# Optimization experiments

Measured on AMD Instinct MI355X. Metric: run time of the kernel, lower is better.

Reference implementation:

```python
import jax, jax.numpy as jnp
import numpy as np

N_NODES = 50000
N_EDGES = 800000
IN_SIZE = 128
HIDDEN = 128   # out_size * 2
OUT_SIZE = 64


def setup_inputs() -> dict:
    key = jax.random.key(0)
    ks = jax.random.split(key, 6)
    h = jax.random.normal(ks[0], (N_NODES, IN_SIZE), dtype=jnp.float32)
    W1 = jax.random.normal(ks[1], (IN_SIZE, HIDDEN), dtype=jnp.float32) * (1.0 / np.sqrt(IN_SIZE))
    b1 = jnp.zeros((HIDDEN,), dtype=jnp.float32)
    W2 = jax.random.normal(ks[2], (HIDDEN, OUT_SIZE), dtype=jnp.float32) * (1.0 / np.sqrt(HIDDEN))
    b2 = jnp.zeros((OUT_SIZE,), dtype=jnp.float32)
    src = jax.random.randint(ks[3], (N_EDGES,), 0, N_NODES, dtype=jnp.int64)
    dst = jax.random.randint(ks[4], (N_EDGES,), 0, N_NODES, dtype=jnp.int64)
    return {"h": h, "W1": W1, "b1": b1, "W2": W2, "b2": b2, "src": src, "dst": dst}


def _norms(src, dst, n_nodes):
    # DGL GraphConv norm='both': scale by out_degree^{-1/2} (src side)
    # and in_degree^{-1/2} (dst side); zero degrees clamped to 1.
    ones = jnp.ones(src.shape, dtype=jnp.float32)
    out_deg = jnp.maximum(jax.ops.segment_sum(ones, src, num_segments=n_nodes), 1.0)
    in_deg = jnp.maximum(jax.ops.segment_sum(ones, dst, num_segments=n_nodes), 1.0)
    return (out_deg ** -0.5)[:, None], (in_deg ** -0.5)[:, None]


def _graph_conv(x, W, b, src, dst, norm_out, norm_in, n_nodes):
    # h' = D_in^{-1/2} A D_out^{-1/2} x W + b
    x = x * norm_out                                   # [N, F]
    agg = jax.ops.segment_sum(x[src], dst, num_segments=n_nodes)  # SpMM: [N, F]
    return (agg * norm_in) @ W + b


def reference(h, W1, b1, W2, b2, src, dst):
    n_nodes = h.shape[0]
    norm_out, norm_in = _norms(src, dst, n_nodes)
    h = jax.nn.relu(_graph_conv(h, W1, b1, src, dst, norm_out, norm_in, n_nodes))
    h = jax.nn.relu(_graph_conv(h, W2, b2, src, dst, norm_out, norm_in, n_nodes))
    return h
```

## Files before the change

### kernel.cpp

```cpp
#include <hip/hip_runtime.h>

#define N_NODES 50000
#define N_EDGES 800000
#define IN_SIZE 128
#define HIDDEN 128
#define OUT_SIZE 64

#define CHUNKS 128
#define CHUNK_EDGES 6250
#define NBS 196
#define GA_BLOCKS 391

typedef __attribute__((ext_vector_type(8))) short bf16x8;
typedef __attribute__((ext_vector_type(4))) float f32x4;

static __device__ inline unsigned short bf16_rne(float x) {
    unsigned ua = __float_as_uint(x);
    return (unsigned short)((ua + 0x7fffu + ((ua >> 16) & 1u)) >> 16);
}

static __device__ inline unsigned short f16_bits(float x) {
    _Float16 hx = (_Float16)x;
    return __builtin_bit_cast(unsigned short, hx);
}

static __device__ inline unsigned pack_f16x2(float a, float b) {
    return (unsigned)f16_bits(a) | ((unsigned)f16_bits(b) << 16);
}

static __device__ inline float2 unpack_f16x2(unsigned u) {
    _Float16 lo = __builtin_bit_cast(_Float16, (unsigned short)(u & 0xffffu));
    _Float16 hi = __builtin_bit_cast(_Float16, (unsigned short)(u >> 16));
    return make_float2((float)lo, (float)hi);
}

__global__ __launch_bounds__(256) void wpack_kernel(const float* __restrict__ W1,
                                                    const float* __restrict__ W2,
                                                    unsigned short* __restrict__ wf_hi,
                                                    unsigned short* __restrict__ wf_lo,
                                                    unsigned short* __restrict__ wf2_hi,
                                                    unsigned short* __restrict__ wf2_lo) {
    int idx = blockIdx.x * 256 + threadIdx.x;
    if (idx < 2048) {
        int l  = idx & 63;
        int ct = (idx >> 6) & 7;
        int ks = idx >> 9;
        int col = ct * 16 + (l & 15);
        int k0  = ks * 32 + (l >> 4) * 8;
        unsigned short hi[8], lo[8];
        #pragma unroll
        for (int j = 0; j < 8; ++j) {
            float x = W1[(size_t)(k0 + j) * 128 + col];
            unsigned short h16 = bf16_rne(x);
            hi[j] = h16;
            lo[j] = bf16_rne(x - __uint_as_float((unsigned)h16 << 16));
        }
        ((uint4*)wf_hi)[idx] = *(const uint4*)hi;
        ((uint4*)wf_lo)[idx] = *(const uint4*)lo;
    } else if (idx < 3072) {
        int i2 = idx - 2048;
        int l  = i2 & 63;
        int ct = (i2 >> 6) & 3;
        int ks = i2 >> 8;
        int col = ct * 16 + (l & 15);
        int k0  = ks * 32 + (l >> 4) * 8;
        unsigned short hi[8], lo[8];
        #pragma unroll
        for (int j = 0; j < 8; ++j) {
            float x = W2[(size_t)(k0 + j) * 64 + col];
            unsigned short h16 = bf16_rne(x);
            hi[j] = h16;
            lo[j] = bf16_rne(x - __uint_as_float((unsigned)h16 << 16));
        }
        ((uint4*)wf2_hi)[i2] = *(const uint4*)hi;
        ((uint4*)wf2_lo)[i2] = *(const uint4*)lo;
    }
}

__global__ __launch_bounds__(256) void gemmA_kernel(const float* __restrict__ h,
                                                    const unsigned short* __restrict__ wf_hi,
                                                    const unsigned short* __restrict__ wf_lo,
                                                    const float* __restrict__ norm_out,
                                                    unsigned short* __restrict__ t1) {
    const int t  = threadIdx.x;
    const int wv = t >> 6;
    const int l  = t & 63;
    const int lrow = l & 15;
    const int g    = l >> 4;
    const int n0 = blockIdx.x * 128 + wv * 32;

    int r0 = n0 + lrow;      if (r0 > N_NODES - 1) r0 = N_NODES - 1;
    int r1 = n0 + 16 + lrow; if (r1 > N_NODES - 1) r1 = N_NODES - 1;
    const float* h0 = h + (size_t)r0 * 128 + g * 8;
    const float* h1 = h + (size_t)r1 * 128 + g * 8;

    f32x4 acc[2][8];
    #pragma unroll
    for (int rt = 0; rt < 2; ++rt)
        #pragma unroll
        for (int ct = 0; ct < 8; ++ct)
            acc[rt][ct] = (f32x4){0.f, 0.f, 0.f, 0.f};

    const bf16x8* bh_base = (const bf16x8*)wf_hi;
    const bf16x8* bl_base = (const bf16x8*)wf_lo;

    for (int ks = 0; ks < 4; ++ks) {
        float a0[8], a1[8];
        *(float4*)(a0)     = *(const float4*)(h0 + ks * 32);
        *(float4*)(a0 + 4) = *(const float4*)(h0 + ks * 32 + 4);
        *(float4*)(a1)     = *(const float4*)(h1 + ks * 32);
        *(float4*)(a1 + 4) = *(const float4*)(h1 + ks * 32 + 4);

        bf16x8 a0h, a0l, a1h, a1l;
        #pragma unroll
        for (int j = 0; j < 8; ++j) {
            unsigned short hh = bf16_rne(a0[j]);
            a0h[j] = (short)hh;
            a0l[j] = (short)bf16_rne(a0[j] - __uint_as_float((unsigned)hh << 16));
            unsigned short h2 = bf16_rne(a1[j]);
            a1h[j] = (short)h2;
            a1l[j] = (short)bf16_rne(a1[j] - __uint_as_float((unsigned)h2 << 16));
        }

        #pragma unroll
        for (int ct = 0; ct < 8; ++ct) {
            const int fi = (ks * 8 + ct) * 64 + l;
            bf16x8 bh = bh_base[fi];
            bf16x8 bl = bl_base[fi];
            acc[0][ct] = __builtin_amdgcn_mfma_f32_16x16x32_bf16(a0l, bh, acc[0][ct], 0, 0, 0);
            acc[0][ct] = __builtin_amdgcn_mfma_f32_16x16x32_bf16(a0h, bl, acc[0][ct], 0, 0, 0);
            acc[0][ct] = __builtin_amdgcn_mfma_f32_16x16x32_bf16(a0h, bh, acc[0][ct], 0, 0, 0);
            acc[1][ct] = __builtin_amdgcn_mfma_f32_16x16x32_bf16(a1l, bh, acc[1][ct], 0, 0, 0);
            acc[1][ct] = __builtin_amdgcn_mfma_f32_16x16x32_bf16(a1h, bl, acc[1][ct], 0, 0, 0);
            acc[1][ct] = __builtin_amdgcn_mfma_f32_16x16x32_bf16(a1h, bh, acc[1][ct], 0, 0, 0);
        }
    }

    #pragma unroll
    for (int rt = 0; rt < 2; ++rt) {
        float no_[4];
        #pragma unroll
        for (int r = 0; r < 4; ++r) {
            int row = n0 + rt * 16 + g * 4 + r;
            no_[r] = (row < N_NODES) ? norm_out[row] : 0.f;
        }
        #pragma unroll
        for (int ct = 0; ct < 8; ++ct) {
            #pragma unroll
            for (int r = 0; r < 4; ++r) {
                int row = n0 + rt * 16 + g * 4 + r;
                if (row < N_NODES)
                    t1[(size_t)row * 128 + ct * 16 + lrow] = bf16_rne(acc[rt][ct][r] * no_[r]);
            }
        }
    }
}

__global__ __launch_bounds__(256) void gemmB_kernel(const float* __restrict__ h1p,
                                                    const unsigned short* __restrict__ wf2_hi,
                                                    const unsigned short* __restrict__ wf2_lo,
                                                    unsigned short* __restrict__ t2h) {
    const int t  = threadIdx.x;
    const int wv = t >> 6;
    const int l  = t & 63;
    const int lrow = l & 15;
    const int g    = l >> 4;
    const int n0 = blockIdx.x * 128 + wv * 32;

    int r0 = n0 + lrow;      if (r0 > N_NODES - 1) r0 = N_NODES - 1;
    int r1 = n0 + 16 + lrow; if (r1 > N_NODES - 1) r1 = N_NODES - 1;
    const float* h0 = h1p + (size_t)r0 * 128 + g * 8;
    const float* h1 = h1p + (size_t)r1 * 128 + g * 8;

    f32x4 acc[2][4];
    #pragma unroll
    for (int rt = 0; rt < 2; ++rt)
        #pragma unroll
        for (int ct = 0; ct < 4; ++ct)
            acc[rt][ct] = (f32x4){0.f, 0.f, 0.f, 0.f};

    const bf16x8* bh_base = (const bf16x8*)wf2_hi;
    const bf16x8* bl_base = (const bf16x8*)wf2_lo;

    for (int ks = 0; ks < 4; ++ks) {
        float a0[8], a1[8];
        *(float4*)(a0)     = *(const float4*)(h0 + ks * 32);
        *(float4*)(a0 + 4) = *(const float4*)(h0 + ks * 32 + 4);
        *(float4*)(a1)     = *(const float4*)(h1 + ks * 32);
        *(float4*)(a1 + 4) = *(const float4*)(h1 + ks * 32 + 4);

        bf16x8 a0h, a0l, a1h, a1l;
        #pragma unroll
        for (int j = 0; j < 8; ++j) {
            unsigned short hh = bf16_rne(a0[j]);
            a0h[j] = (short)hh;
            a0l[j] = (short)bf16_rne(a0[j] - __uint_as_float((unsigned)hh << 16));
            unsigned short h2 = bf16_rne(a1[j]);
            a1h[j] = (short)h2;
            a1l[j] = (short)bf16_rne(a1[j] - __uint_as_float((unsigned)h2 << 16));
        }

        #pragma unroll
        for (int ct = 0; ct < 4; ++ct) {
            const int fi = (ks * 4 + ct) * 64 + l;
            bf16x8 bh = bh_base[fi];
            bf16x8 bl = bl_base[fi];
            acc[0][ct] = __builtin_amdgcn_mfma_f32_16x16x32_bf16(a0l, bh, acc[0][ct], 0, 0, 0);
            acc[0][ct] = __builtin_amdgcn_mfma_f32_16x16x32_bf16(a0h, bl, acc[0][ct], 0, 0, 0);
            acc[0][ct] = __builtin_amdgcn_mfma_f32_16x16x32_bf16(a0h, bh, acc[0][ct], 0, 0, 0);
            acc[1][ct] = __builtin_amdgcn_mfma_f32_16x16x32_bf16(a1l, bh, acc[1][ct], 0, 0, 0);
            acc[1][ct] = __builtin_amdgcn_mfma_f32_16x16x32_bf16(a1h, bl, acc[1][ct], 0, 0, 0);
            acc[1][ct] = __builtin_amdgcn_mfma_f32_16x16x32_bf16(a1h, bh, acc[1][ct], 0, 0, 0);
        }
    }

    #pragma unroll
    for (int rt = 0; rt < 2; ++rt) {
        #pragma unroll
        for (int ct = 0; ct < 4; ++ct) {
            #pragma unroll
            for (int r = 0; r < 4; ++r) {
                int row = n0 + rt * 16 + g * 4 + r;
                if (row < N_NODES)
                    t2h[(size_t)row * 64 + ct * 16 + lrow] = f16_bits(acc[rt][ct][r]);
            }
        }
    }
}

__global__ __launch_bounds__(1024) void hist_kernel(const int* __restrict__ src,
                                                    const int* __restrict__ dst,
                                                    unsigned char* __restrict__ cntD,
                                                    unsigned char* __restrict__ cntS,
                                                    unsigned char* __restrict__ rp) {
    __shared__ unsigned hD[12500];
    __shared__ unsigned hS[12500];
    const int t = threadIdx.x;
    const int c = blockIdx.x;

    for (int i = t; i < 12500; i += 1024) { hD[i] = 0u; hS[i] = 0u; }
    __syncthreads();

    const int base = c * CHUNK_EDGES;
    for (int i = t; i < CHUNK_EDGES; i += 1024) {
        int e = base + i;
        int d = dst[e];
        int s = src[e];
        unsigned shd = (unsigned)(d & 3) * 8u;
        unsigned old = atomicAdd(&hD[d >> 2], 1u << shd);
        rp[e] = (unsigned char)((old >> shd) & 0xffu);
        atomicAdd(&hS[s >> 2], 1u << ((unsigned)(s & 3) * 8u));
    }
    __syncthreads();

    unsigned* gD = (unsigned*)cntD + (size_t)c * 12500;
    unsigned* gS = (unsigned*)cntS + (size_t)c * 12500;
    for (int i = t; i < 12500; i += 1024) { gD[i] = hD[i]; gS[i] = hS[i]; }
}

__global__ __launch_bounds__(256) void deg_scan_kernel(unsigned char* __restrict__ cntD,
                                                       const unsigned char* __restrict__ cntS,
                                                       int* __restrict__ row_ptr,
                                                       int* __restrict__ bsum,
                                                       float* __restrict__ norm_out,
                                                       float* __restrict__ norm_in) {
    const int t = threadIdx.x, lane = t & 63, w = t >> 6;
    const int n = blockIdx.x * 256 + t;
    unsigned sumD = 0u, sumS = 0u;
    if (n < N_NODES) {
        #pragma unroll 4
        for (int c = 0; c < CHUNKS; ++c) {
            size_t idx = (size_t)c * 50000 + n;
            unsigned v = cntD[idx];
            cntD[idx] = (unsigned char)sumD;
            sumD += v;
            sumS += cntS[idx];
        }
        norm_in[n]  = rsqrtf((float)(sumD ? sumD : 1u));
        norm_out[n] = rsqrtf((float)(sumS ? sumS : 1u));
    }
    __shared__ int wsum[4];
    int v = (n < N_NODES) ? (int)sumD : 0;
    int incl = v;
    #pragma unroll
    for (int d = 1; d < 64; d <<= 1) {
        int u = __shfl_up(incl, d, 64);
        if (lane >= d) incl += u;
    }
    if (lane == 63) wsum[w] = incl;
    __syncthreads();
    int woff = 0, total = 0;
    #pragma unroll
    for (int j = 0; j < 4; ++j) {
        int s = wsum[j];
        if (j < w) woff += s;
        total += s;
    }
    if (n < N_NODES) row_ptr[n] = woff + incl - v;
    if (t == 0) bsum[blockIdx.x] = total;
}

__global__ __launch_bounds__(64) void scan2_kernel(int* __restrict__ bsum,
                                                   int* __restrict__ row_ptr) {
    const int lane = threadIdx.x;
    int carry = 0;
    for (int base = 0; base < NBS; base += 64) {
        int t = base + lane;
        int v = (t < NBS) ? bsum[t] : 0;
        int incl = v;
        #pragma unroll
        for (int d = 1; d < 64; d <<= 1) {
            int u = __shfl_up(incl, d, 64);
            if (lane >= d) incl += u;
        }
        int excl = carry + incl - v;
        if (t < NBS) bsum[t] = excl;
        if (t == NBS - 1) row_ptr[N_NODES] = N_EDGES - excl;
        carry += __shfl(incl, 63, 64);
    }
}

__global__ __launch_bounds__(256) void place_kernel(const int* __restrict__ src,
                                                    const int* __restrict__ dst,
                                                    const int* __restrict__ row_ptr,
                                                    const int* __restrict__ bsum,
                                                    const unsigned char* __restrict__ cntD,
                                                    const unsigned char* __restrict__ rp,
                                                    int* __restrict__ eidx) {
    int e = blockIdx.x * 256 + threadIdx.x;
    if (e < N_EDGES) {
        int d = dst[e];
        int c = e / CHUNK_EDGES;
        int pos = row_ptr[d] + bsum[d >> 8] + (int)cntD[(size_t)c * 50000 + d] + (int)rp[e];
        eidx[pos] = src[e];
    }
}

__global__ __launch_bounds__(256) void pull128_kernel(const unsigned short* __restrict__ xb,
                                                      const int* __restrict__ row_ptr,
                                                      const int* __restrict__ bsum,
                                                      const int* __restrict__ eidx,
                                                      const float* __restrict__ b1,
                                                      const float* __restrict__ norm_in,
                                                      const float* __restrict__ norm_out,
                                                      float* __restrict__ out) {
    int node = blockIdx.x * 4 + (threadIdx.x >> 6);
    node = __builtin_amdgcn_readfirstlane(node);
    const int lane = threadIdx.x & 63;
    const int beg = __builtin_amdgcn_readfirstlane(row_ptr[node] + bsum[node >> 8]);
    const int end = __builtin_amdgcn_readfirstlane(row_ptr[node + 1] + bsum[(node + 1) >> 8]);

    float2 acc0 = make_float2(0.f, 0.f);
    float2 acc1 = make_float2(0.f, 0.f);
    float2 acc2 = make_float2(0.f, 0.f);
    float2 acc3 = make_float2(0.f, 0.f);

    for (int base = beg; base < end; base += 64) {
        const int cnt = min(64, end - base);
        int my_e = (lane < cnt) ? eidx[base + lane] : 0;
        int k = 0;
        for (; k + 7 < cnt; k += 8) {
            int s0 = __builtin_amdgcn_readlane(my_e, k);
            int s1 = __builtin_amdgcn_readlane(my_e, k + 1);
            int s2 = __builtin_amdgcn_readlane(my_e, k + 2);
            int s3 = __builtin_amdgcn_readlane(my_e, k + 3);
            int s4 = __builtin_amdgcn_readlane(my_e, k + 4);
            int s5 = __builtin_amdgcn_readlane(my_e, k + 5);
            int s6 = __builtin_amdgcn_readlane(my_e, k + 6);
            int s7 = __builtin_amdgcn_readlane(my_e, k + 7);
            unsigned u0 = ((const unsigned*)(xb + (size_t)s0 * 128))[lane];
            unsigned u1 = ((const unsigned*)(xb + (size_t)s1 * 128))[lane];
            unsigned u2 = ((const unsigned*)(xb + (size_t)s2 * 128))[lane];
            unsigned u3 = ((const unsigned*)(xb + (size_t)s3 * 128))[lane];
            unsigned u4 = ((const unsigned*)(xb + (size_t)s4 * 128))[lane];
            unsigned u5 = ((const unsigned*)(xb + (size_t)s5 * 128))[lane];
            unsigned u6 = ((const unsigned*)(xb + (size_t)s6 * 128))[lane];
            unsigned u7 = ((const unsigned*)(xb + (size_t)s7 * 128))[lane];
            acc0.x += __uint_as_float(u0 << 16);
            acc0.y += __uint_as_float(u0 & 0xffff0000u);
            acc1.x += __uint_as_float(u1 << 16);
            acc1.y += __uint_as_float(u1 & 0xffff0000u);
            acc2.x += __uint_as_float(u2 << 16);
            acc2.y += __uint_as_float(u2 & 0xffff0000u);
            acc3.x += __uint_as_float(u3 << 16);
            acc3.y += __uint_as_float(u3 & 0xffff0000u);
            acc0.x += __uint_as_float(u4 << 16);
            acc0.y += __uint_as_float(u4 & 0xffff0000u);
            acc1.x += __uint_as_float(u5 << 16);
            acc1.y += __uint_as_float(u5 & 0xffff0000u);
            acc2.x += __uint_as_float(u6 << 16);
            acc2.y += __uint_as_float(u6 & 0xffff0000u);
            acc3.x += __uint_as_float(u7 << 16);
            acc3.y += __uint_as_float(u7 & 0xffff0000u);
        }
        for (; k + 3 < cnt; k += 4) {
            int s0 = __builtin_amdgcn_readlane(my_e, k);
            int s1 = __builtin_amdgcn_readlane(my_e, k + 1);
            int s2 = __builtin_amdgcn_readlane(my_e, k + 2);
            int s3 = __builtin_amdgcn_readlane(my_e, k + 3);
            unsigned u0 = ((const unsigned*)(xb + (size_t)s0 * 128))[lane];
            unsigned u1 = ((const unsigned*)(xb + (size_t)s1 * 128))[lane];
            unsigned u2 = ((const unsigned*)(xb + (size_t)s2 * 128))[lane];
            unsigned u3 = ((const unsigned*)(xb + (size_t)s3 * 128))[lane];
            acc0.x += __uint_as_float(u0 << 16);
            acc0.y += __uint_as_float(u0 & 0xffff0000u);
            acc1.x += __uint_as_float(u1 << 16);
            acc1.y += __uint_as_float(u1 & 0xffff0000u);
            acc2.x += __uint_as_float(u2 << 16);
            acc2.y += __uint_as_float(u2 & 0xffff0000u);
            acc3.x += __uint_as_float(u3 << 16);
            acc3.y += __uint_as_float(u3 & 0xffff0000u);
        }
        for (; k < cnt; ++k) {
            int s0 = __builtin_amdgcn_readlane(my_e, k);
            unsigned u0 = ((const unsigned*)(xb + (size_t)s0 * 128))[lane];
            acc0.x += __uint_as_float(u0 << 16);
            acc0.y += __uint_as_float(u0 & 0xffff0000u);
        }
    }

    float ni = norm_in[node];
    float no = norm_out[node];
    float2 bb = ((const float2*)b1)[lane];
    float sx = (acc0.x + acc1.x) + (acc2.x + acc3.x);
    float sy = (acc0.y + acc1.y) + (acc2.y + acc3.y);
    float2 r;
    r.x = fmaxf(fmaf(sx, ni, bb.x), 0.f) * no;
    r.y = fmaxf(fmaf(sy, ni, bb.y), 0.f) * no;
    ((float2*)(out + (size_t)node * 128))[lane] = r;
}

__global__ __launch_bounds__(256) void pull64_kernel(const unsigned* __restrict__ x,
                                                     const int* __restrict__ row_ptr,
                                                     const int* __restrict__ bsum,
                                                     const int* __restrict__ eidx,
                                                     const float* __restrict__ b2,
                                                     const float* __restrict__ norm_in,
                                                     float* __restrict__ out) {
    int node = blockIdx.x * 4 + (threadIdx.x >> 6);
    node = __builtin_amdgcn_readfirstlane(node);
    const int lane = threadIdx.x & 63;
    const int half = lane >> 5;
    const int fl = lane & 31;
    const int beg = __builtin_amdgcn_readfirstlane(row_ptr[node] + bsum[node >> 8]);
    const int end = __builtin_amdgcn_readfirstlane(row_ptr[node + 1] + bsum[(node + 1) >> 8]);

    float2 a0 = make_float2(0.f, 0.f);
    float2 a1 = make_float2(0.f, 0.f);
    float2 a2 = make_float2(0.f, 0.f);
    float2 a3 = make_float2(0.f, 0.f);

    for (int base = beg; base < end; base += 64) {
        const int cnt = min(64, end - base);
        int my_e = (lane < cnt) ? eidx[base + lane] : 0;
        int k = 0;
        for (; k + 7 < cnt; k += 8) {
            int sa0 = __builtin_amdgcn_readlane(my_e, k);
            int sb0 = __builtin_amdgcn_readlane(my_e, k + 1);
            int sa1 = __builtin_amdgcn_readlane(my_e, k + 2);
            int sb1 = __builtin_amdgcn_readlane(my_e, k + 3);
            int sa2 = __builtin_amdgcn_readlane(my_e, k + 4);
            int sb2 = __builtin_amdgcn_readlane(my_e, k + 5);
            int sa3 = __builtin_amdgcn_readlane(my_e, k + 6);
            int sb3 = __builtin_amdgcn_readlane(my_e, k + 7);
            int e0 = half ? sb0 : sa0;
            int e1 = half ? sb1 : sa1;
            int e2 = half ? sb2 : sa2;
            int e3 = half ? sb3 : sa3;
            unsigned u0 = x[(size_t)e0 * 32 + fl];
            unsigned u1 = x[(size_t)e1 * 32 + fl];
            unsigned u2 = x[(size_t)e2 * 32 + fl];
            unsigned u3 = x[(size_t)e3 * 32 + fl];
            float2 v0 = unpack_f16x2(u0);
            float2 v1 = unpack_f16x2(u1);
            float2 v2 = unpack_f16x2(u2);
            float2 v3 = unpack_f16x2(u3);
            a0.x += v0.x; a0.y += v0.y;
            a1.x += v1.x; a1.y += v1.y;
            a2.x += v2.x; a2.y += v2.y;
            a3.x += v3.x; a3.y += v3.y;
        }
        for (; k + 1 < cnt; k += 2) {
            int sa = __builtin_amdgcn_readlane(my_e, k);
            int sb = __builtin_amdgcn_readlane(my_e, k + 1);
            int e0 = half ? sb : sa;
            unsigned u = x[(size_t)e0 * 32 + fl];
            float2 v = unpack_f16x2(u);
            a0.x += v.x; a0.y += v.y;
        }
        if (k < cnt) {
            int sa = __builtin_amdgcn_readlane(my_e, k);
            if (half == 0) {
                unsigned u = x[(size_t)sa * 32 + fl];
                float2 v = unpack_f16x2(u);
                a0.x += v.x; a0.y += v.y;
            }
        }
    }

    float ax = (a0.x + a1.x) + (a2.x + a3.x);
    float ay = (a0.y + a1.y) + (a2.y + a3.y);
    ax += __shfl_xor(ax, 32, 64);
    ay += __shfl_xor(ay, 32, 64);
    if (half == 0) {
        float ni = norm_in[node];
        float2 bb = ((const float2*)b2)[fl];
        float2 r;
        r.x = fmaxf(fmaf(ax, ni, bb.x), 0.f);
        r.y = fmaxf(fmaf(ay, ni, bb.y), 0.f);
        ((float2*)(out + (size_t)node * 64))[fl] = r;
    }
}

extern "C" void kernel_launch(void* const* d_in, const int* in_sizes, int n_in,
                              void* d_out, int out_size, void* d_ws, size_t ws_size,
                              hipStream_t stream) {
    const float* h  = (const float*)d_in[0];
    const float* W1 = (const float*)d_in[1];
    const float* b1 = (const float*)d_in[2];
    const float* W2 = (const float*)d_in[3];
    const float* b2 = (const float*)d_in[4];
    const int* src  = (const int*)d_in[5];
    const int* dst  = (const int*)d_in[6];
    float* out = (float*)d_out;

    char* ws = (char*)d_ws;
    size_t off = 0;
    auto alloc = [&](size_t bytes) {
        void* p = ws + off;
        off = (off + bytes + 255) & ~(size_t)255;
        return p;
    };
    float* norm_out   = (float*)alloc(N_NODES * sizeof(float));
    float* norm_in    = (float*)alloc(N_NODES * sizeof(float));
    int* row_ptr      = (int*)alloc((N_NODES + 1) * sizeof(int));
    int* bsum         = (int*)alloc(NBS * sizeof(int));
    unsigned short* wf_hi  = (unsigned short*)alloc(2048 * 16);
    unsigned short* wf_lo  = (unsigned short*)alloc(2048 * 16);
    unsigned short* wf2_hi = (unsigned short*)alloc(1024 * 16);
    unsigned short* wf2_lo = (unsigned short*)alloc(1024 * 16);
    int* eidx         = (int*)alloc((size_t)N_EDGES * sizeof(int));
    unsigned short* t1 = (unsigned short*)alloc((size_t)N_NODES * 128 * sizeof(short));
    float* h1p        = (float*)alloc((size_t)N_NODES * 128 * sizeof(float));

    unsigned char* cntD = (unsigned char*)h1p;
    unsigned char* cntS = cntD + (size_t)CHUNKS * 50000;
    unsigned char* rp   = cntS + (size_t)CHUNKS * 50000;
    unsigned short* t2h = t1;

    wpack_kernel<<<12, 256, 0, stream>>>(W1, W2, wf_hi, wf_lo, wf2_hi, wf2_lo);

    hist_kernel<<<CHUNKS, 1024, 0, stream>>>(src, dst, cntD, cntS, rp);

    deg_scan_kernel<<<NBS, 256, 0, stream>>>(cntD, cntS, row_ptr, bsum, norm_out, norm_in);

    scan2_kernel<<<1, 64, 0, stream>>>(bsum, row_ptr);

    place_kernel<<<(N_EDGES + 255) / 256, 256, 0, stream>>>(src, dst, row_ptr, bsum, cntD, rp, eidx);

    gemmA_kernel<<<GA_BLOCKS, 256, 0, stream>>>(h, wf_hi, wf_lo, norm_out, t1);

    pull128_kernel<<<N_NODES / 4, 256, 0, stream>>>(t1, row_ptr, bsum, eidx, b1,
                                                    norm_in, norm_out, h1p);

    gemmB_kernel<<<GA_BLOCKS, 256, 0, stream>>>(h1p, wf2_hi, wf2_lo, t2h);
    pull64_kernel<<<N_NODES / 4, 256, 0, stream>>>((const unsigned*)t2h, row_ptr, bsum, eidx,
                                                   b2, norm_in, out);
}
```

Baseline: 212.0 us.

## Merge post-histogram stages into one cooperative persistent kernel with grid syncs

Replaces the chain of small kernel launches (weight pack, degree scan, scan2, place, gemmA, pull128, gemmB, pull64) with one cooperative persistent kernel. Grid-wide syncs separate the dependent phases, and blocks loop over virtual block indices. Independent work is placed in the same phase (weight pack with degree scan, gemmA with edge placement) so they overlap. This removes launch gaps and tail effects, but adds grid-sync cost and may lower occupancy because the fused kernel's register use is set by its heaviest body.

After: 581.5 us. 2.74x slower.

```diff
diff --git a/kernel.cpp b/kernel.cpp
--- a/kernel.cpp
+++ b/kernel.cpp
@@ -1,15 +1,16 @@
 #include <hip/hip_runtime.h>
+#include <hip/hip_cooperative_groups.h>
+
+namespace cg = cooperative_groups;
 
 #define N_NODES 50000
 #define N_EDGES 800000
-#define IN_SIZE 128
-#define HIDDEN 128
-#define OUT_SIZE 64
-
 #define CHUNKS 128
 #define CHUNK_EDGES 6250
 #define NBS 196
 #define GA_BLOCKS 391
+#define PLACE_BLOCKS 3125
+#define PULL_BLOCKS 12500
 
 typedef __attribute__((ext_vector_type(8))) short bf16x8;
 typedef __attribute__((ext_vector_type(4))) float f32x4;
@@ -22,10 +23,6 @@
 static __device__ inline unsigned short f16_bits(float x) {
     _Float16 hx = (_Float16)x;
     return __builtin_bit_cast(unsigned short, hx);
-}
-
-static __device__ inline unsigned pack_f16x2(float a, float b) {
-    return (unsigned)f16_bits(a) | ((unsigned)f16_bits(b) << 16);
 }
 
 static __device__ inline float2 unpack_f16x2(unsigned u) {
@@ -34,13 +31,65 @@
     return make_float2((float)lo, (float)hi);
 }
 
-__global__ __launch_bounds__(256) void wpack_kernel(const float* __restrict__ W1,
-                                                    const float* __restrict__ W2,
-                                                    unsigned short* __restrict__ wf_hi,
-                                                    unsigned short* __restrict__ wf_lo,
-                                                    unsigned short* __restrict__ wf2_hi,
-                                                    unsigned short* __restrict__ wf2_lo) {
-    int idx = blockIdx.x * 256 + threadIdx.x;
+struct MegaArgs {
+    const float* h;
+    const float* W1;
+    const float* b1;
+    const float* W2;
+    const float* b2;
+    unsigned char* cntD;
+    const unsigned char* cntS;
+    const unsigned char* rp;
+    const int* src;
+    const int* dst;
+    int* row_ptr;
+    int* bsum;
+    float* norm_out;
+    float* norm_in;
+    unsigned short* wf_hi;
+    unsigned short* wf_lo;
+    unsigned short* wf2_hi;
+    unsigned short* wf2_lo;
+    int* eidx;
+    unsigned short* t1;
+    float* h1p;
+    unsigned short* t2h;
+    float* out;
+};
+
+__global__ __launch_bounds__(1024) void hist_kernel(const int* __restrict__ src,
+                                                    const int* __restrict__ dst,
+                                                    unsigned char* __restrict__ cntD,
+                                                    unsigned char* __restrict__ cntS,
+                                                    unsigned char* __restrict__ rp) {
+    __shared__ unsigned hD[12500];
+    __shared__ unsigned hS[12500];
+    const int t = threadIdx.x;
+    const int c = blockIdx.x;
+
+    for (int i = t; i < 12500; i += 1024) { hD[i] = 0u; hS[i] = 0u; }
+    __syncthreads();
+
+    const int base = c * CHUNK_EDGES;
+    for (int i = t; i < CHUNK_EDGES; i += 1024) {
+        int e = base + i;
+        int d = dst[e];
+        int s = src[e];
+        unsigned shd = (unsigned)(d & 3) * 8u;
+        unsigned old = atomicAdd(&hD[d >> 2], 1u << shd);
+        rp[e] = (unsigned char)((old >> shd) & 0xffu);
+        atomicAdd(&hS[s >> 2], 1u << ((unsigned)(s & 3) * 8u));
+    }
+    __syncthreads();
+
+    unsigned* gD = (unsigned*)cntD + (size_t)c * 12500;
+    unsigned* gS = (unsigned*)cntS + (size_t)c * 12500;
+    for (int i = t; i < 12500; i += 1024) { gD[i] = hD[i]; gS[i] = hS[i]; }
+}
+
+
+static __device__ void wpack_body(int vb, const MegaArgs& a) {
+    int idx = vb * 256 + threadIdx.x;
     if (idx < 2048) {
         int l  = idx & 63;
         int ct = (idx >> 6) & 7;
@@ -50,13 +99,13 @@
         unsigned short hi[8], lo[8];
         #pragma unroll
         for (int j = 0; j < 8; ++j) {
-            float x = W1[(size_t)(k0 + j) * 128 + col];
+            float x = a.W1[(size_t)(k0 + j) * 128 + col];
             unsigned short h16 = bf16_rne(x);
             hi[j] = h16;
             lo[j] = bf16_rne(x - __uint_as_float((unsigned)h16 << 16));
         }
-        ((uint4*)wf_hi)[idx] = *(const uint4*)hi;
-        ((uint4*)wf_lo)[idx] = *(const uint4*)lo;
+        ((uint4*)a.wf_hi)[idx] = *(const uint4*)hi;
+        ((uint4*)a.wf_lo)[idx] = *(const uint4*)lo;
     } else if (idx < 3072) {
         int i2 = idx - 2048;
         int l  = i2 & 63;
@@ -67,32 +116,95 @@
         unsigned short hi[8], lo[8];
         #pragma unroll
         for (int j = 0; j < 8; ++j) {
-            float x = W2[(size_t)(k0 + j) * 64 + col];
+            float x = a.W2[(size_t)(k0 + j) * 64 + col];
             unsigned short h16 = bf16_rne(x);
             hi[j] = h16;
             lo[j] = bf16_rne(x - __uint_as_float((unsigned)h16 << 16));
         }
-        ((uint4*)wf2_hi)[i2] = *(const uint4*)hi;
-        ((uint4*)wf2_lo)[i2] = *(const uint4*)lo;
-    }
-}
-
-__global__ __launch_bounds__(256) void gemmA_kernel(const float* __restrict__ h,
-                                                    const unsigned short* __restrict__ wf_hi,
-                                                    const unsigned short* __restrict__ wf_lo,
-                                                    const float* __restrict__ norm_out,
-                                                    unsigned short* __restrict__ t1) {
+        ((uint4*)a.wf2_hi)[i2] = *(const uint4*)hi;
+        ((uint4*)a.wf2_lo)[i2] = *(const uint4*)lo;
+    }
+}
+
+static __device__ void deg_scan_body(int vb, const MegaArgs& a, int* wsum) {
+    const int t = threadIdx.x, lane = t & 63, w = t >> 6;
+    const int n = vb * 256 + t;
+    unsigned sumD = 0u, sumS = 0u;
+    if (n < N_NODES) {
+        #pragma unroll 4
+        for (int c = 0; c < CHUNKS; ++c) {
+            size_t idx = (size_t)c * 50000 + n;
+            unsigned v = a.cntD[idx];
+            a.cntD[idx] = (unsigned char)sumD;
+            sumD += v;
+            sumS += a.cntS[idx];
+        }
+        a.norm_in[n]  = rsqrtf((float)(sumD ? sumD : 1u));
+        a.norm_out[n] = rsqrtf((float)(sumS ? sumS : 1u));
+    }
+    int v = (n < N_NODES) ? (int)sumD : 0;
+    int incl = v;
+    #pragma unroll
+    for (int d = 1; d < 64; d <<= 1) {
+        int u = __shfl_up(incl, d, 64);
+        if (lane >= d) incl += u;
+    }
+    if (lane == 63) wsum[w] = incl;
+    __syncthreads();
+    int woff = 0, total = 0;
+    #pragma unroll
+    for (int j = 0; j < 4; ++j) {
+        int s = wsum[j];
+        if (j < w) woff += s;
+        total += s;
+    }
+    __syncthreads();
+    if (n < N_NODES) a.row_ptr[n] = woff + incl - v;
+    if (t == 0) a.bsum[vb] = total;
+}
+
+static __device__ void scan2_body(const MegaArgs& a) {
+    const int lane = threadIdx.x;
+    int carry = 0;
+    for (int base = 0; base < NBS; base += 64) {
+        int t = base + lane;
+        int v = (t < NBS) ? a.bsum[t] : 0;
+        int incl = v;
+        #pragma unroll
+        for (int d = 1; d < 64; d <<= 1) {
+            int u = __shfl_up(incl, d, 64);
+            if (lane >= d) incl += u;
+        }
+        int excl = carry + incl - v;
+        if (t < NBS) a.bsum[t] = excl;
+        if (t == NBS - 1) a.row_ptr[N_NODES] = N_EDGES - excl;
+        carry += __shfl(incl, 63, 64);
+    }
+}
+
+static __device__ void place_body(int vb, const MegaArgs& a) {
+    int e = vb * 256 + threadIdx.x;
+    if (e < N_EDGES) {
+        int d = a.dst[e];
+        int c = e / CHUNK_EDGES;
+        int pos = a.row_ptr[d] + a.bsum[d >> 8] + (int)a.cntD[(size_t)c * 50000 + d]
+                + (int)a.rp[e];
+        a.eidx[pos] = a.src[e];
+    }
+}
+
+static __device__ void gemmA_body(int vb, const MegaArgs& a) {
     const int t  = threadIdx.x;
     const int wv = t >> 6;
     const int l  = t & 63;
     const int lrow = l & 15;
     const int g    = l >> 4;
-    const int n0 = blockIdx.x * 128 + wv * 32;
+    const int n0 = vb * 128 + wv * 32;
 
     int r0 = n0 + lrow;      if (r0 > N_NODES - 1) r0 = N_NODES - 1;
     int r1 = n0 + 16 + lrow; if (r1 > N_NODES - 1) r1 = N_NODES - 1;
-    const float* h0 = h + (size_t)r0 * 128 + g * 8;
-    const float* h1 = h + (size_t)r1 * 128 + g * 8;
+    const float* h0 = a.h + (size_t)r0 * 128 + g * 8;
+    const float* h1 = a.h + (size_t)r1 * 128 + g * 8;
 
     f32x4 acc[2][8];
     #pragma unroll
@@ -101,8 +213,8 @@
         for (int ct = 0; ct < 8; ++ct)
             acc[rt][ct] = (f32x4){0.f, 0.f, 0.f, 0.f};
 
-    const bf16x8* bh_base = (const bf16x8*)wf_hi;
-    const bf16x8* bl_base = (const bf16x8*)wf_lo;
+    const bf16x8* bh_base = (const bf16x8*)a.wf_hi;
+    const bf16x8* bl_base = (const bf16x8*)a.wf_lo;
 
     for (int ks = 0; ks < 4; ++ks) {
         float a0[8], a1[8];
@@ -142,7 +254,7 @@
         #pragma unroll
         for (int r = 0; r < 4; ++r) {
             int row = n0 + rt * 16 + g * 4 + r;
-            no_[r] = (row < N_NODES) ? norm_out[row] : 0.f;
+            no_[r] = (row < N_NODES) ? a.norm_out[row] : 0.f;
         }
         #pragma unroll
         for (int ct = 0; ct < 8; ++ct) {
@@ -150,27 +262,24 @@
             for (int r = 0; r < 4; ++r) {
                 int row = n0 + rt * 16 + g * 4 + r;
                 if (row < N_NODES)
-                    t1[(size_t)row * 128 + ct * 16 + lrow] = bf16_rne(acc[rt][ct][r] * no_[r]);
+                    a.t1[(size_t)row * 128 + ct * 16 + lrow] = bf16_rne(acc[rt][ct][r] * no_[r]);
             }
         }
     }
 }
 
-__global__ __launch_bounds__(256) void gemmB_kernel(const float* __restrict__ h1p,
-                                                    const unsigned short* __restrict__ wf2_hi,
-                                                    const unsigned short* __restrict__ wf2_lo,
-                                                    unsigned short* __restrict__ t2h) {
+static __device__ void gemmB_body(int vb, const MegaArgs& a) {
     const int t  = threadIdx.x;
     const int wv = t >> 6;
     const int l  = t & 63;
     const int lrow = l & 15;
     const int g    = l >> 4;
-    const int n0 = blockIdx.x * 128 + wv * 32;
+    const int n0 = vb * 128 + wv * 32;
 
     int r0 = n0 + lrow;      if (r0 > N_NODES - 1) r0 = N_NODES - 1;
     int r1 = n0 + 16 + lrow; if (r1 > N_NODES - 1) r1 = N_NODES - 1;
-    const float* h0 = h1p + (size_t)r0 * 128 + g * 8;
-    const float* h1 = h1p + (size_t)r1 * 128 + g * 8;
+    const float* h0 = a.h1p + (size_t)r0 * 128 + g * 8;
+    const float* h1 = a.h1p + (size_t)r1 * 128 + g * 8;
 
     f32x4 acc[2][4];
     #pragma unroll
@@ -179,8 +288,8 @@
         for (int ct = 0; ct < 4; ++ct)
             acc[rt][ct] = (f32x4){0.f, 0.f, 0.f, 0.f};
 
-    const bf16x8* bh_base = (const bf16x8*)wf2_hi;
-    const bf16x8* bl_base = (const bf16x8*)wf2_lo;
+    const bf16x8* bh_base = (const bf16x8*)a.wf2_hi;
+    const bf16x8* bl_base = (const bf16x8*)a.wf2_lo;
 
     for (int ks = 0; ks < 4; ++ks) {
         float a0[8], a1[8];
@@ -222,133 +331,19 @@
             for (int r = 0; r < 4; ++r) {
                 int row = n0 + rt * 16 + g * 4 + r;
                 if (row < N_NODES)
-                    t2h[(size_t)row * 64 + ct * 16 + lrow] = f16_bits(acc[rt][ct][r]);
+                    a.t2h[(size_t)row * 64 + ct * 16 + lrow] = f16_bits(acc[rt][ct][r]);
             }
         }
     }
 }
 
-__global__ __launch_bounds__(1024) void hist_kernel(const int* __restrict__ src,
-                                                    const int* __restrict__ dst,
-                                                    unsigned char* __restrict__ cntD,
-                                                    unsigned char* __restrict__ cntS,
-                                                    unsigned char* __restrict__ rp) {
-    __shared__ unsigned hD[12500];
-    __shared__ unsigned hS[12500];
-    const int t = threadIdx.x;
-    const int c = blockIdx.x;
-
-    for (int i = t; i < 12500; i += 1024) { hD[i] = 0u; hS[i] = 0u; }
-    __syncthreads();
-
-    const int base = c * CHUNK_EDGES;
-    for (int i = t; i < CHUNK_EDGES; i += 1024) {
-        int e = base + i;
-        int d = dst[e];
-        int s = src[e];
-        unsigned shd = (unsigned)(d & 3) * 8u;
-        unsigned old = atomicAdd(&hD[d >> 2], 1u << shd);
-        rp[e] = (unsigned char)((old >> shd) & 0xffu);
-        atomicAdd(&hS[s >> 2], 1u << ((unsigned)(s & 3) * 8u));
-    }
-    __syncthreads();
-
-    unsigned* gD = (unsigned*)cntD + (size_t)c * 12500;
-    unsigned* gS = (unsigned*)cntS + (size_t)c * 12500;
-    for (int i = t; i < 12500; i += 1024) { gD[i] = hD[i]; gS[i] = hS[i]; }
-}
-
-__global__ __launch_bounds__(256) void deg_scan_kernel(unsigned char* __restrict__ cntD,
-                                                       const unsigned char* __restrict__ cntS,
-                                                       int* __restrict__ row_ptr,
-                                                       int* __restrict__ bsum,
-                                                       float* __restrict__ norm_out,
-                                                       float* __restrict__ norm_in) {
-    const int t = threadIdx.x, lane = t & 63, w = t >> 6;
-    const int n = blockIdx.x * 256 + t;
-    unsigned sumD = 0u, sumS = 0u;
-    if (n < N_NODES) {
-        #pragma unroll 4
-        for (int c = 0; c < CHUNKS; ++c) {
-            size_t idx = (size_t)c * 50000 + n;
-            unsigned v = cntD[idx];
-            cntD[idx] = (unsigned char)sumD;
-            sumD += v;
-            sumS += cntS[idx];
-        }
-        norm_in[n]  = rsqrtf((float)(sumD ? sumD : 1u));
-        norm_out[n] = rsqrtf((float)(sumS ? sumS : 1u));
-    }
-    __shared__ int wsum[4];
-    int v = (n < N_NODES) ? (int)sumD : 0;
-    int incl = v;
-    #pragma unroll
-    for (int d = 1; d < 64; d <<= 1) {
-        int u = __shfl_up(incl, d, 64);
-        if (lane >= d) incl += u;
-    }
-    if (lane == 63) wsum[w] = incl;
-    __syncthreads();
-    int woff = 0, total = 0;
-    #pragma unroll
-    for (int j = 0; j < 4; ++j) {
-        int s = wsum[j];
-        if (j < w) woff += s;
-        total += s;
-    }
-    if (n < N_NODES) row_ptr[n] = woff + incl - v;
-    if (t == 0) bsum[blockIdx.x] = total;
-}
-
-__global__ __launch_bounds__(64) void scan2_kernel(int* __restrict__ bsum,
-                                                   int* __restrict__ row_ptr) {
-    const int lane = threadIdx.x;
-    int carry = 0;
-    for (int base = 0; base < NBS; base += 64) {
-        int t = base + lane;
-        int v = (t < NBS) ? bsum[t] : 0;
-        int incl = v;
-        #pragma unroll
-        for (int d = 1; d < 64; d <<= 1) {
-            int u = __shfl_up(incl, d, 64);
-            if (lane >= d) incl += u;
-        }
-        int excl = carry + incl - v;
-        if (t < NBS) bsum[t] = excl;
-        if (t == NBS - 1) row_ptr[N_NODES] = N_EDGES - excl;
-        carry += __shfl(incl, 63, 64);
-    }
-}
-
-__global__ __launch_bounds__(256) void place_kernel(const int* __restrict__ src,
-                                                    const int* __restrict__ dst,
-                                                    const int* __restrict__ row_ptr,
-                                                    const int* __restrict__ bsum,
-                                                    const unsigned char* __restrict__ cntD,
-                                                    const unsigned char* __restrict__ rp,
-                                                    int* __restrict__ eidx) {
-    int e = blockIdx.x * 256 + threadIdx.x;
-    if (e < N_EDGES) {
-        int d = dst[e];
-        int c = e / CHUNK_EDGES;
-        int pos = row_ptr[d] + bsum[d >> 8] + (int)cntD[(size_t)c * 50000 + d] + (int)rp[e];
-        eidx[pos] = src[e];
-    }
-}
-
-__global__ __launch_bounds__(256) void pull128_kernel(const unsigned short* __restrict__ xb,
-                                                      const int* __restrict__ row_ptr,
-                                                      const int* __restrict__ bsum,
-                                                      const int* __restrict__ eidx,
-                                                      const float* __restrict__ b1,
-                                                      const float* __restrict__ norm_in,
-                                                      const float* __restrict__ norm_out,
-                                                      float* __restrict__ out) {
-    int node = blockIdx.x * 4 + (threadIdx.x >> 6);
+static __device__ void pull128_body(int vb, const MegaArgs& a) {
+    int node = vb * 4 + (threadIdx.x >> 6);
     node = __builtin_amdgcn_readfirstlane(node);
     const int lane = threadIdx.x & 63;
-    const int beg = __builtin_amdgcn_readfirstlane(row_ptr[node] + bsum[node >> 8]);
-    const int end = __builtin_amdgcn_readfirstlane(row_ptr[node + 1] + bsum[(node + 1) >> 8]);
+    const unsigned short* xb = a.t1;
+    const int beg = __builtin_amdgcn_readfirstlane(a.row_ptr[node] + a.bsum[node >> 8]);
+    const int end = __builtin_amdgcn_readfirstlane(a.row_ptr[node + 1] + a.bsum[(node + 1) >> 8]);
 
     float2 acc0 = make_float2(0.f, 0.f);
     float2 acc1 = make_float2(0.f, 0.f);
@@ -357,7 +352,7 @@
 
     for (int base = beg; base < end; base += 64) {
         const int cnt = min(64, end - base);
-        int my_e = (lane < cnt) ? eidx[base + lane] : 0;
+        int my_e = (lane < cnt) ? a.eidx[base + lane] : 0;
         int k = 0;
         for (; k + 7 < cnt; k += 8) {
             int s0 = __builtin_amdgcn_readlane(my_e, k);
@@ -419,31 +414,26 @@
         }
     }
 
-    float ni = norm_in[node];
-    float no = norm_out[node];
-    float2 bb = ((const float2*)b1)[lane];
+    float ni = a.norm_in[node];
+    float no = a.norm_out[node];
+    float2 bb = ((const float2*)a.b1)[lane];
     float sx = (acc0.x + acc1.x) + (acc2.x + acc3.x);
     float sy = (acc0.y + acc1.y) + (acc2.y + acc3.y);
     float2 r;
     r.x = fmaxf(fmaf(sx, ni, bb.x), 0.f) * no;
     r.y = fmaxf(fmaf(sy, ni, bb.y), 0.f) * no;
-    ((float2*)(out + (size_t)node * 128))[lane] = r;
-}
-
-__global__ __launch_bounds__(256) void pull64_kernel(const unsigned* __restrict__ x,
-                                                     const int* __restrict__ row_ptr,
-                                                     const int* __restrict__ bsum,
-                                                     const int* __restrict__ eidx,
-                                                     const float* __restrict__ b2,
-                                                     const float* __restrict__ norm_in,
-                                                     float* __restrict__ out) {
-    int node = blockIdx.x * 4 + (threadIdx.x >> 6);
+    ((float2*)(a.h1p + (size_t)node * 128))[lane] = r;
+}
+
+static __device__ void pull64_body(int vb, const MegaArgs& a) {
+    int node = vb * 4 + (threadIdx.x >> 6);
     node = __builtin_amdgcn_readfirstlane(node);
     const int lane = threadIdx.x & 63;
     const int half = lane >> 5;
     const int fl = lane & 31;
-    const int beg = __builtin_amdgcn_readfirstlane(row_ptr[node] + bsum[node >> 8]);
-    const int end = __builtin_amdgcn_readfirstlane(row_ptr[node + 1] + bsum[(node + 1) >> 8]);
+    const unsigned* x = (const unsigned*)a.t2h;
+    const int beg = __builtin_amdgcn_readfirstlane(a.row_ptr[node] + a.bsum[node >> 8]);
+    const int end = __builtin_amdgcn_readfirstlane(a.row_ptr[node + 1] + a.bsum[(node + 1) >> 8]);
 
     float2 a0 = make_float2(0.f, 0.f);
     float2 a1 = make_float2(0.f, 0.f);
@@ -452,7 +442,7 @@
 
     for (int base = beg; base < end; base += 64) {
         const int cnt = min(64, end - base);
-        int my_e = (lane < cnt) ? eidx[base + lane] : 0;
+        int my_e = (lane < cnt) ? a.eidx[base + lane] : 0;
         int k = 0;
         for (; k + 7 < cnt; k += 8) {
             int sa0 = __builtin_amdgcn_readlane(my_e, k);
@@ -503,13 +493,42 @@
     ax += __shfl_xor(ax, 32, 64);
     ay += __shfl_xor(ay, 32, 64);
     if (half == 0) {
-        float ni = norm_in[node];
-        float2 bb = ((const float2*)b2)[fl];
+        float ni = a.norm_in[node];
+        float2 bb = ((const float2*)a.b2)[fl];
         float2 r;
         r.x = fmaxf(fmaf(ax, ni, bb.x), 0.f);
         r.y = fmaxf(fmaf(ay, ni, bb.y), 0.f);
-        ((float2*)(out + (size_t)node * 64))[fl] = r;
-    }
+        ((float2*)(a.out + (size_t)node * 64))[fl] = r;
+    }
+}
+
+__global__ __launch_bounds__(256, 4) void mega_kernel(MegaArgs a) {
+    cg::grid_group grid = cg::this_grid();
+    __shared__ int wsum[4];
+    const int nb = gridDim.x;
+
+    for (int vb = blockIdx.x; vb < 12 + NBS; vb += nb) {
+        if (vb < 12) wpack_body(vb, a);
+        else deg_scan_body(vb - 12, a, wsum);
+    }
+    grid.sync();
+
+    if (blockIdx.x == 0 && threadIdx.x < 64) scan2_body(a);
+    grid.sync();
+
+    for (int vb = blockIdx.x; vb < GA_BLOCKS + PLACE_BLOCKS; vb += nb) {
+        if (vb < GA_BLOCKS) gemmA_body(vb, a);
+        else place_body(vb - GA_BLOCKS, a);
+    }
+    grid.sync();
+
+    for (int vb = blockIdx.x; vb < PULL_BLOCKS; vb += nb) pull128_body(vb, a);
+    grid.sync();
+
+    for (int vb = blockIdx.x; vb < GA_BLOCKS; vb += nb) gemmB_body(vb, a);
+    grid.sync();
+
+    for (int vb = blockIdx.x; vb < PULL_BLOCKS; vb += nb) pull64_body(vb, a);
 }
 
 extern "C" void kernel_launch(void* const* d_in, const int* in_sizes, int n_in,
@@ -548,22 +567,23 @@
     unsigned char* rp   = cntS + (size_t)CHUNKS * 50000;
     unsigned short* t2h = t1;
 
-    wpack_kernel<<<12, 256, 0, stream>>>(W1, W2, wf_hi, wf_lo, wf2_hi, wf2_lo);
-
     hist_kernel<<<CHUNKS, 1024, 0, stream>>>(src, dst, cntD, cntS, rp);
 
-    deg_scan_kernel<<<NBS, 256, 0, stream>>>(cntD, cntS, row_ptr, bsum, norm_out, norm_in);
-
-    scan2_kernel<<<1, 64, 0, stream>>>(bsum, row_ptr);
-
-    place_kernel<<<(N_EDGES + 255) / 256, 256, 0, stream>>>(src, dst, row_ptr, bsum, cntD, rp, eidx);
-
-    gemmA_kernel<<<GA_BLOCKS, 256, 0, stream>>>(h, wf_hi, wf_lo, norm_out, t1);
-
-    pull128_kernel<<<N_NODES / 4, 256, 0, stream>>>(t1, row_ptr, bsum, eidx, b1,
-                                                    norm_in, norm_out, h1p);
-
-    gemmB_kernel<<<GA_BLOCKS, 256, 0, stream>>>(h1p, wf2_hi, wf2_lo, t2h);
-    pull64_kernel<<<N_NODES / 4, 256, 0, stream>>>((const unsigned*)t2h, row_ptr, bsum, eidx,
-                                                   b2, norm_in, out);
-}
+    MegaArgs ma;
+    ma.h = h; ma.W1 = W1; ma.b1 = b1; ma.W2 = W2; ma.b2 = b2;
+    ma.cntD = cntD; ma.cntS = cntS; ma.rp = rp;
+    ma.src = src; ma.dst = dst;
+    ma.row_ptr = row_ptr; ma.bsum = bsum;
+    ma.norm_out = norm_out; ma.norm_in = norm_in;
+    ma.wf_hi = wf_hi; ma.wf_lo = wf_lo; ma.wf2_hi = wf2_hi; ma.wf2_lo = wf2_lo;
+    ma.eidx = eidx; ma.t1 = t1; ma.h1p = h1p; ma.t2h = t2h; ma.out = out;
+
+    int bpc = 0;
+    if (hipOccupancyMaxActiveBlocksPerMultiprocessor(&bpc, mega_kernel, 256, 0) != hipSuccess
+        || bpc < 1) bpc = 2;
+    int nblk = bpc * 256;
+    if (nblk > 1024) nblk = 1024;
+
+    void* kargs[] = { (void*)&ma };
+    hipLaunchCooperativeKernel((void*)mega_kernel, dim3(nblk), dim3(256), kargs, 0, stream);
+}
```
